# Kernel optimization log

Measured on AMD Instinct MI355X. Metric: run time of the kernel, lower is better.

Reference implementation:

```python
import jax, jax.numpy as jnp
import numpy as np

N_NODES = 50000
N_EDGES = 800000
D_IN = 256
D_HID = 256
D_OUT = 256
BN_EPS = 1e-5
NORM_EPS = 1e-12


def _glorot(key, out_dim, in_dim):
    a = np.sqrt(6.0 / (in_dim + out_dim)).astype(np.float32)
    return jax.random.uniform(key, (out_dim, in_dim), jnp.float32, -a, a)


def setup_inputs() -> dict:
    key = jax.random.key(0)
    ks = jax.random.split(key, 8)
    x = jax.random.normal(ks[0], (N_NODES, D_IN), jnp.float32)
    edge_index = jax.random.randint(ks[1], (2, N_EDGES), 0, N_NODES, dtype=jnp.int32)
    batch = jnp.zeros((N_NODES,), jnp.int32)
    return {
        "x": x,
        "W1_l": _glorot(ks[2], D_HID, D_IN),
        "b1_l": jnp.zeros((D_HID,), jnp.float32),
        "W1_r": _glorot(ks[3], D_HID, D_IN),
        "W2_l": _glorot(ks[4], D_OUT, D_HID),
        "b2_l": jnp.zeros((D_OUT,), jnp.float32),
        "W2_r": _glorot(ks[5], D_OUT, D_HID),
        "gamma1": jnp.ones((D_HID,), jnp.float32),
        "beta1": jnp.zeros((D_HID,), jnp.float32),
        "edge_index": edge_index,
        "batch": batch,
    }


def _sage_conv(x, W_l, b_l, W_r, src, dst, n_nodes):
    # PyG SAGEConv (aggr='mean'): out = lin_l(mean_j x_j) + lin_r(x)
    msgs = x[src]                                            # [E, d] gather
    s = jax.ops.segment_sum(msgs, dst, num_segments=n_nodes)  # [N, d] scatter-add
    cnt = jax.ops.segment_sum(jnp.ones((src.shape[0], 1), x.dtype), dst,
                              num_segments=n_nodes)
    agg = jnp.where(cnt > 0, s / jnp.maximum(cnt, 1.0), 0.0)
    return agg @ W_l.T + b_l + x @ W_r.T


def _batch_norm(h, gamma, beta):
    mu = jnp.mean(h, axis=0)
    var = jnp.mean((h - mu) ** 2, axis=0)  # biased, as torch train-mode BN
    return (h - mu) * jax.lax.rsqrt(var + BN_EPS) * gamma + beta


def _l2_normalize(h):
    n = jnp.linalg.norm(h, axis=-1, keepdims=True)
    return h / jnp.maximum(n, NORM_EPS)


def reference(x, W1_l, b1_l, W1_r, W2_l, b2_l, W2_r, gamma1, beta1,
              edge_index, batch):
    n = x.shape[0]
    src, dst = edge_index[0], edge_index[1]
    # layer 1: SAGEConv -> BN (train stats) -> ReLU (dropout = identity in eval)
    h = _sage_conv(x, W1_l, b1_l, W1_r, src, dst, n)
    h = jax.nn.relu(_batch_norm(h, gamma1, beta1))
    # layer 2: SAGEConv -> L2 normalize
    h = _sage_conv(h, W2_l, b2_l, W2_r, src, dst, n)
    node_emb = _l2_normalize(h)
    # global mean pool over batch ids (single graph here), then normalize
    gsum = jax.ops.segment_sum(node_emb, batch, num_segments=1)
    gcnt = jax.ops.segment_sum(jnp.ones((n, 1), node_emb.dtype), batch,
                               num_segments=1)
    graph_emb = _l2_normalize(gsum / jnp.maximum(gcnt, 1.0))
    return node_emb, graph_emb
```

## Files before the change

### kernel.cpp

```cpp
#include <hip/hip_runtime.h>
#include <math.h>

#define NN 50000
#define NE 800000
#define D  256
#define SCB 196
#define NB2 391

typedef unsigned short u16;
typedef __attribute__((ext_vector_type(8))) short short8;
typedef __attribute__((ext_vector_type(8))) unsigned short u16x8;
typedef __attribute__((ext_vector_type(4))) float f32x4;

__device__ __forceinline__ u16 f2b(float f) {
    unsigned u = __float_as_uint(f);
    return (u16)((u + 0x7FFFu + ((u >> 16) & 1u)) >> 16);
}
__device__ __forceinline__ float b2f(u16 b) {
    return __uint_as_float(((unsigned)b) << 16);
}

__device__ __forceinline__ void gl16(const u16* g, u16* l) {
    __builtin_amdgcn_global_load_lds(
        (const __attribute__((address_space(1))) void*)g,
        (__attribute__((address_space(3))) void*)l, 16, 0, 0);
}

__global__ void wxconv_kernel(const float* __restrict__ x,
                              const float* __restrict__ W1l, const float* __restrict__ W1r,
                              const float* __restrict__ W2l, const float* __restrict__ W2r,
                              const int* __restrict__ dst,
                              u16* __restrict__ Acat,
                              u16* __restrict__ Wcat1, u16* __restrict__ Wcat2,
                              int* __restrict__ deg) {
    int b = blockIdx.x;
    if (b < 12500) {
        int idx = b * 256 + threadIdx.x;
        int r = idx >> 6;
        int c4 = (idx & 63) * 4;
        float4 v = *(const float4*)&x[(size_t)r * 256 + c4];
        ushort4 o;
        o.x = f2b(v.x); o.y = f2b(v.y); o.z = f2b(v.z); o.w = f2b(v.w);
        *(ushort4*)&Acat[(size_t)r * 512 + 256 + c4] = o;
    } else if (b < 12756) {
        int r = b - 12500;
        int j = threadIdx.x;
        Wcat1[r * 512 + j]       = f2b(W1l[r * 256 + j]);
        Wcat1[r * 512 + 256 + j] = f2b(W1r[r * 256 + j]);
        Wcat2[r * 512 + j]       = f2b(W2l[r * 256 + j]);
        Wcat2[r * 512 + 256 + j] = f2b(W2r[r * 256 + j]);
    } else {
        int e0 = ((b - 12756) * 256 + threadIdx.x) * 4;
        if (e0 + 3 < NE) {
            int4 d = *(const int4*)&dst[e0];
            atomicAdd(&deg[d.x], 1);
            atomicAdd(&deg[d.y], 1);
            atomicAdd(&deg[d.z], 1);
            atomicAdd(&deg[d.w], 1);
        } else {
            for (int e = e0; e < NE; e++) atomicAdd(&deg[dst[e]], 1);
        }
    }
}

__global__ void scanA_kernel(const int* __restrict__ deg, int* __restrict__ partial) {
    int t = threadIdx.x;
    int i = blockIdx.x * 256 + t;
    int v = (i < NN) ? deg[i] : 0;
#pragma unroll
    for (int o = 32; o; o >>= 1) v += __shfl_xor(v, o);
    __shared__ int sm[4];
    if ((t & 63) == 0) sm[t >> 6] = v;
    __syncthreads();
    if (t == 0) partial[blockIdx.x] = sm[0] + sm[1] + sm[2] + sm[3];
}

__global__ void scanB_kernel(const int* __restrict__ partial, int* __restrict__ base,
                             int* __restrict__ offs) {
    __shared__ int sm[256];
    int t = threadIdx.x;
    int v = (t < SCB) ? partial[t] : 0;
    sm[t] = v;
    __syncthreads();
    for (int off = 1; off < 256; off <<= 1) {
        int u = 0;
        if (t >= off) u = sm[t - off];
        __syncthreads();
        sm[t] += u;
        __syncthreads();
    }
    if (t < SCB) base[t] = sm[t] - v;
    if (t == 255) offs[NN] = sm[255];
}

__global__ void scanC_kernel(const int* __restrict__ deg, const int* __restrict__ base,
                             int* __restrict__ offs, int* __restrict__ cur) {
    __shared__ int sm[256];
    int t = threadIdx.x;
    int i = blockIdx.x * 256 + t;
    int v = (i < NN) ? deg[i] : 0;
    sm[t] = v;
    __syncthreads();
    for (int off = 1; off < 256; off <<= 1) {
        int u = 0;
        if (t >= off) u = sm[t - off];
        __syncthreads();
        sm[t] += u;
        __syncthreads();
    }
    int o = base[blockIdx.x] + sm[t] - v;
    if (i < NN) {
        offs[i] = o;
        cur[i] = o;
    }
}

__global__ void fill_kernel(const int* __restrict__ src, const int* __restrict__ dst,
                            int* __restrict__ cur, int* __restrict__ csr) {
    int e0 = (blockIdx.x * blockDim.x + threadIdx.x) * 8;
    if (e0 + 7 < NE) {
        int4 d0 = *(const int4*)&dst[e0];
        int4 d1 = *(const int4*)&dst[e0 + 4];
        int4 s0 = *(const int4*)&src[e0];
        int4 s1 = *(const int4*)&src[e0 + 4];
        int p0 = atomicAdd(&cur[d0.x], 1);
        int p1 = atomicAdd(&cur[d0.y], 1);
        int p2 = atomicAdd(&cur[d0.z], 1);
        int p3 = atomicAdd(&cur[d0.w], 1);
        int p4 = atomicAdd(&cur[d1.x], 1);
        int p5 = atomicAdd(&cur[d1.y], 1);
        int p6 = atomicAdd(&cur[d1.z], 1);
        int p7 = atomicAdd(&cur[d1.w], 1);
        csr[p0] = s0.x; csr[p1] = s0.y; csr[p2] = s0.z; csr[p3] = s0.w;
        csr[p4] = s1.x; csr[p5] = s1.y; csr[p6] = s1.z; csr[p7] = s1.w;
    } else {
        for (int e = e0; e < NE; e++) {
            int pos = atomicAdd(&cur[dst[e]], 1);
            csr[pos] = src[e];
        }
    }
}

__global__ __launch_bounds__(256)
void agg_kernel(const u16* __restrict__ Acat, const int* __restrict__ csr,
                const int* __restrict__ offs, u16* __restrict__ AcatW) {
    int wid = (blockIdx.x * blockDim.x + threadIdx.x) >> 6;
    int lane = threadIdx.x & 63;
    if (wid >= NN) return;
    int beg = offs[wid];
    int end = offs[wid + 1];
    int deg = end - beg;
    int half = lane >> 5;
    int lc = (lane & 31) * 8;
    int mid = beg + ((deg + 1) >> 1);
    int e  = half ? mid : beg;
    int hi = half ? end : mid;
    float a[8] = {0.f, 0.f, 0.f, 0.f, 0.f, 0.f, 0.f, 0.f};
    for (; e + 7 < hi; e += 8) {
        int s0 = csr[e + 0], s1 = csr[e + 1], s2 = csr[e + 2], s3 = csr[e + 3];
        int s4 = csr[e + 4], s5 = csr[e + 5], s6 = csr[e + 6], s7 = csr[e + 7];
        u16x8 v0 = *(const u16x8*)&Acat[(size_t)s0 * 512 + 256 + lc];
        u16x8 v1 = *(const u16x8*)&Acat[(size_t)s1 * 512 + 256 + lc];
        u16x8 v2 = *(const u16x8*)&Acat[(size_t)s2 * 512 + 256 + lc];
        u16x8 v3 = *(const u16x8*)&Acat[(size_t)s3 * 512 + 256 + lc];
        u16x8 v4 = *(const u16x8*)&Acat[(size_t)s4 * 512 + 256 + lc];
        u16x8 v5 = *(const u16x8*)&Acat[(size_t)s5 * 512 + 256 + lc];
        u16x8 v6 = *(const u16x8*)&Acat[(size_t)s6 * 512 + 256 + lc];
        u16x8 v7 = *(const u16x8*)&Acat[(size_t)s7 * 512 + 256 + lc];
#pragma unroll
        for (int i = 0; i < 8; i++)
            a[i] += ((b2f(v0[i]) + b2f(v1[i])) + (b2f(v2[i]) + b2f(v3[i]))) +
                    ((b2f(v4[i]) + b2f(v5[i])) + (b2f(v6[i]) + b2f(v7[i])));
    }
    for (; e + 3 < hi; e += 4) {
        int s0 = csr[e + 0], s1 = csr[e + 1], s2 = csr[e + 2], s3 = csr[e + 3];
        u16x8 v0 = *(const u16x8*)&Acat[(size_t)s0 * 512 + 256 + lc];
        u16x8 v1 = *(const u16x8*)&Acat[(size_t)s1 * 512 + 256 + lc];
        u16x8 v2 = *(const u16x8*)&Acat[(size_t)s2 * 512 + 256 + lc];
        u16x8 v3 = *(const u16x8*)&Acat[(size_t)s3 * 512 + 256 + lc];
#pragma unroll
        for (int i = 0; i < 8; i++)
            a[i] += (b2f(v0[i]) + b2f(v1[i])) + (b2f(v2[i]) + b2f(v3[i]));
    }
    for (; e < hi; e++) {
        int s0 = csr[e];
        u16x8 v0 = *(const u16x8*)&Acat[(size_t)s0 * 512 + 256 + lc];
#pragma unroll
        for (int i = 0; i < 8; i++) a[i] += b2f(v0[i]);
    }
#pragma unroll
    for (int i = 0; i < 8; i++) a[i] += __shfl_xor(a[i], 32);
    float sc = (deg > 0) ? 1.0f / (float)deg : 0.0f;
    if (half == 0) {
        u16x8 o;
#pragma unroll
        for (int i = 0; i < 8; i++) o[i] = f2b(a[i] * sc);
        *(u16x8*)&AcatW[(size_t)wid * 512 + lc] = o;
    }
}

__global__ __launch_bounds__(256)
void mfma_gemm_kernel(const u16* __restrict__ A, const u16* __restrict__ W,
                      const float* __restrict__ bias, u16* __restrict__ Cout) {
    __shared__ u16 As[4][128 * 32];
    __shared__ u16 Bs[4][128 * 32];
    const int tid = threadIdx.x;
    const int l = tid & 63;
    const int wid = tid >> 6;
    const int wr = wid >> 1, wc = wid & 1;
    const int row0 = blockIdx.x * 128;
    const int col0 = blockIdx.y * 128;

    const u16* aptr[2];
    const u16* bptr[2];
#pragma unroll
    for (int i = 0; i < 2; i++) {
        int row = wid * 32 + i * 16 + (l >> 2);
        int kg = (l & 3) ^ ((row >> 1) & 3);
        int ra = row0 + row;
        if (ra > NN - 1) ra = NN - 1;
        aptr[i] = A + (size_t)ra * 512 + kg * 8;
        bptr[i] = W + (size_t)(col0 + row) * 512 + kg * 8;
    }

    f32x4 acc[4][4] = {};

#define STAGE1(b, t)                                                         \
    do {                                                                     \
        _Pragma("unroll") for (int i_ = 0; i_ < 2; i_++) {                   \
            gl16(aptr[i_] + (t) * 32, &As[b][(wid * 32 + i_ * 16) * 32]);    \
            gl16(bptr[i_] + (t) * 32, &Bs[b][(wid * 32 + i_ * 16) * 32]);    \
        }                                                                    \
    } while (0)

    STAGE1(0, 0);
    STAGE1(1, 1);

    const int kq = l >> 4;
    const int sw = ((l & 15) >> 1) & 3;
#pragma unroll
    for (int t = 0; t < 16; t++) {
        if (t + 2 < 16) STAGE1((t + 2) & 3, t + 2);

        if (t < 14)       asm volatile("s_waitcnt vmcnt(8)" ::: "memory");
        else if (t == 14) asm volatile("s_waitcnt vmcnt(4)" ::: "memory");
        else              asm volatile("s_waitcnt vmcnt(0)" ::: "memory");
        __builtin_amdgcn_s_barrier();
        __builtin_amdgcn_sched_barrier(0);

        short8 af[4], bf[4];
#pragma unroll
        for (int m = 0; m < 4; m++) {
            int row = wr * 64 + m * 16 + (l & 15);
            af[m] = *(const short8*)&As[t & 3][row * 32 + (kq ^ sw) * 8];
        }
#pragma unroll
        for (int n = 0; n < 4; n++) {
            int row = wc * 64 + n * 16 + (l & 15);
            bf[n] = *(const short8*)&Bs[t & 3][row * 32 + (kq ^ sw) * 8];
        }
#pragma unroll
        for (int m = 0; m < 4; m++)
#pragma unroll
            for (int n = 0; n < 4; n++)
                acc[m][n] = __builtin_amdgcn_mfma_f32_16x16x32_bf16(
                    af[m], bf[n], acc[m][n], 0, 0, 0);
    }
#undef STAGE1

    const int cq = l >> 4;
    const int cc = l & 15;
#pragma unroll
    for (int m = 0; m < 4; m++) {
#pragma unroll
        for (int n = 0; n < 4; n++) {
            int c = col0 + wc * 64 + n * 16 + cc;
#pragma unroll
            for (int j = 0; j < 4; j++) {
                int r = row0 + wr * 64 + m * 16 + cq * 4 + j;
                if (r < NN)
                    Cout[(size_t)r * 256 + c] = f2b(acc[m][n][j] + bias[c]);
            }
        }
    }
}

__global__ __launch_bounds__(512)
void gemm2_l2_kernel(const u16* __restrict__ A, const u16* __restrict__ W,
                     const float* __restrict__ bias, float* __restrict__ out,
                     float* __restrict__ colsum_part) {
    __shared__ u16 As[3][128 * 32];
    __shared__ u16 Bs[3][256 * 32];
    const int tid = threadIdx.x;
    const int l = tid & 63;
    const int wid = tid >> 6;
    const int wr = wid >> 2;
    const int wc = wid & 3;
    const int row0 = blockIdx.x * 128;

    const u16* aptr;
    const u16* bptr[2];
    {
        int row = wid * 16 + (l >> 2);
        int kg = (l & 3) ^ ((row >> 1) & 3);
        int ra = row0 + row;
        if (ra > NN - 1) ra = NN - 1;
        aptr = A + (size_t)ra * 512 + kg * 8;
    }
#pragma unroll
    for (int i = 0; i < 2; i++) {
        int row = wid * 32 + i * 16 + (l >> 2);
        int kg = (l & 3) ^ ((row >> 1) & 3);
        bptr[i] = W + (size_t)row * 512 + kg * 8;
    }

    f32x4 acc[4][4] = {};

#define STAGE2(b, t)                                                         \
    do {                                                                     \
        gl16(aptr + (t) * 32, &As[b][(wid * 16) * 32]);                      \
        _Pragma("unroll") for (int i_ = 0; i_ < 2; i_++)                     \
            gl16(bptr[i_] + (t) * 32, &Bs[b][(wid * 32 + i_ * 16) * 32]);    \
    } while (0)

    STAGE2(0, 0);
    STAGE2(1, 1);

    const int kq = l >> 4;
    const int sw = ((l & 15) >> 1) & 3;
#pragma unroll
    for (int t = 0; t < 16; t++) {
        if (t < 15) asm volatile("s_waitcnt vmcnt(3)" ::: "memory");
        else        asm volatile("s_waitcnt vmcnt(0)" ::: "memory");
        __builtin_amdgcn_s_barrier();
        __builtin_amdgcn_sched_barrier(0);

        if (t + 2 < 16) STAGE2((t + 2) % 3, t + 2);

        short8 af[4], bf[4];
#pragma unroll
        for (int m = 0; m < 4; m++) {
            int row = wr * 64 + m * 16 + (l & 15);
            af[m] = *(const short8*)&As[t % 3][row * 32 + (kq ^ sw) * 8];
        }
#pragma unroll
        for (int n = 0; n < 4; n++) {
            int row = wc * 64 + n * 16 + (l & 15);
            bf[n] = *(const short8*)&Bs[t % 3][row * 32 + (kq ^ sw) * 8];
        }
#pragma unroll
        for (int m = 0; m < 4; m++)
#pragma unroll
            for (int n = 0; n < 4; n++)
                acc[m][n] = __builtin_amdgcn_mfma_f32_16x16x32_bf16(
                    af[m], bf[n], acc[m][n], 0, 0, 0);
    }
#undef STAGE2

    float* rowsq = (float*)&As[1][0];
    float* colp  = rowsq + 512;
    const int cq = l >> 4;
    const int cc = l & 15;

    float sq[4][4];
#pragma unroll
    for (int m = 0; m < 4; m++)
#pragma unroll
        for (int j = 0; j < 4; j++) {
            float s = 0.f;
#pragma unroll
            for (int n = 0; n < 4; n++) {
                float v = acc[m][n][j] + bias[wc * 64 + n * 16 + cc];
                acc[m][n][j] = v;
                s += v * v;
            }
            sq[m][j] = s;
        }
#pragma unroll
    for (int o = 1; o < 16; o <<= 1)
#pragma unroll
        for (int m = 0; m < 4; m++)
#pragma unroll
            for (int j = 0; j < 4; j++) sq[m][j] += __shfl_xor(sq[m][j], o);

    __syncthreads();
#pragma unroll
    for (int m = 0; m < 4; m++)
#pragma unroll
        for (int j = 0; j < 4; j++)
            if (cc == j) rowsq[wc * 128 + wr * 64 + m * 16 + cq * 4 + j] = sq[m][j];
    __syncthreads();

    float colpart[4] = {0.f, 0.f, 0.f, 0.f};
#pragma unroll
    for (int m = 0; m < 4; m++)
#pragma unroll
        for (int j = 0; j < 4; j++) {
            int rl = wr * 64 + m * 16 + cq * 4 + j;
            float s = rowsq[rl] + rowsq[128 + rl] + rowsq[256 + rl] + rowsq[384 + rl];
            float invn = 1.0f / fmaxf(sqrtf(s), 1e-12f);
            int r = row0 + rl;
            bool ok = (r < NN);
#pragma unroll
            for (int n = 0; n < 4; n++) {
                float vn = acc[m][n][j] * invn;
                if (ok) {
                    out[(size_t)r * 256 + wc * 64 + n * 16 + cc] = vn;
                    colpart[n] += vn;
                }
            }
        }
#pragma unroll
    for (int n = 0; n < 4; n++) {
        colpart[n] += __shfl_xor(colpart[n], 16);
        colpart[n] += __shfl_xor(colpart[n], 32);
    }
    if (l < 16) {
#pragma unroll
        for (int n = 0; n < 4; n++)
            colp[wr * 256 + wc * 64 + n * 16 + l] = colpart[n];
    }
    __syncthreads();
    if (tid < 256)
        colsum_part[(size_t)blockIdx.x * 256 + tid] = colp[tid] + colp[256 + tid];
}

__global__ void colstats_kernel(const u16* __restrict__ h, float* __restrict__ stats) {
    int j = threadIdx.x;
    float s0 = 0.f, s1 = 0.f;
    for (int r = blockIdx.x; r < NN; r += gridDim.x) {
        float v = b2f(h[(size_t)r * 256 + j]);
        s0 += v;
        s1 += v * v;
    }
    atomicAdd(&stats[j], s0);
    atomicAdd(&stats[256 + j], s1);
}

__global__ void bnrelu_kernel(const u16* __restrict__ hb,
                              const float* __restrict__ stats,
                              const float* __restrict__ gamma,
                              const float* __restrict__ beta,
                              u16* __restrict__ Acat) {
    __shared__ float s_scale[256], s_shift[256];
    int t = threadIdx.x;
    {
        const float invN = 1.0f / (float)NN;
        float mu = stats[t] * invN;
        float var = stats[256 + t] * invN - mu * mu;
        float sc = gamma[t] * rsqrtf(var + 1e-5f);
        s_scale[t] = sc;
        s_shift[t] = beta[t] - mu * sc;
    }
    __syncthreads();
    int idx = blockIdx.x * 256 + t;
    int r = idx >> 5;
    int c8 = (idx & 31) * 8;
    u16x8 v = *(const u16x8*)&hb[(size_t)r * 256 + c8];
    u16x8 o;
#pragma unroll
    for (int i = 0; i < 8; i++) {
        float f = b2f(v[i]) * s_scale[c8 + i] + s_shift[c8 + i];
        o[i] = f2b(fmaxf(f, 0.f));
    }
    *(u16x8*)&Acat[(size_t)r * 512 + 256 + c8] = o;
}

__global__ void graph_kernel(const float* __restrict__ colsum_part,
                             float* __restrict__ gout) {
    __shared__ float wsum[4];
    int j = threadIdx.x;
    float s = 0.f;
#pragma unroll 8
    for (int b = 0; b < NB2; b++) s += colsum_part[(size_t)b * 256 + j];
    float v = s * (1.0f / (float)NN);
    float sq = v * v;
#pragma unroll
    for (int o = 32; o; o >>= 1) sq += __shfl_xor(sq, o);
    if ((j & 63) == 0) wsum[j >> 6] = sq;
    __syncthreads();
    float tot = wsum[0] + wsum[1] + wsum[2] + wsum[3];
    gout[j] = v / fmaxf(sqrtf(tot), 1e-12f);
}

extern "C" void kernel_launch(void* const* d_in, const int* in_sizes, int n_in,
                              void* d_out, int out_size, void* d_ws, size_t ws_size,
                              hipStream_t stream) {
    const float* x      = (const float*)d_in[0];
    const float* W1_l   = (const float*)d_in[1];
    const float* b1_l   = (const float*)d_in[2];
    const float* W1_r   = (const float*)d_in[3];
    const float* W2_l   = (const float*)d_in[4];
    const float* b2_l   = (const float*)d_in[5];
    const float* W2_r   = (const float*)d_in[6];
    const float* gamma1 = (const float*)d_in[7];
    const float* beta1  = (const float*)d_in[8];
    const int*   eidx   = (const int*)d_in[9];
    const int* src = eidx;
    const int* dst = eidx + NE;

    char* wsb = (char*)d_ws;
    int*   deg    = (int*)(wsb + 0);
    int*   offs   = (int*)(wsb + 200000);
    int*   cur    = (int*)(wsb + 400004);
    int*   csr    = (int*)(wsb + 600004);
    float* cspart = (float*)(wsb + 600004);
    int*   part   = (int*)(wsb + 3800064);
    int*   base   = (int*)(wsb + 3801088);
    float* stats  = (float*)(wsb + 3802112);
    u16*   Wcat1  = (u16*)(wsb + 3807232);
    u16*   Wcat2  = (u16*)(wsb + 4069376);
    u16*   hb     = (u16*)(wsb + 4331520);
    u16*   Acat   = (u16*)(wsb + 29931520);
    float* out    = (float*)d_out;
    float* gout   = out + (size_t)NN * 256;

    hipMemsetAsync(deg, 0, NN * sizeof(int), stream);
    hipMemsetAsync(stats, 0, 2048, stream);

    const int DEGB = (NE / 4 + 255) / 256;
    wxconv_kernel<<<12756 + DEGB, 256, 0, stream>>>(x, W1_l, W1_r, W2_l, W2_r,
                                                    dst, Acat, Wcat1, Wcat2, deg);

    scanA_kernel<<<SCB, 256, 0, stream>>>(deg, part);
    scanB_kernel<<<1, 256, 0, stream>>>(part, base, offs);
    scanC_kernel<<<SCB, 256, 0, stream>>>(deg, base, offs, cur);
    fill_kernel<<<(NE / 8 + 255) / 256, 256, 0, stream>>>(src, dst, cur, csr);

    dim3 ggrid(NB2, 2);

    agg_kernel<<<12500, 256, 0, stream>>>(Acat, csr, offs, Acat);
    mfma_gemm_kernel<<<ggrid, 256, 0, stream>>>(Acat, Wcat1, b1_l, hb);
    colstats_kernel<<<512, 256, 0, stream>>>(hb, stats);
    bnrelu_kernel<<<6250, 256, 0, stream>>>(hb, stats, gamma1, beta1, Acat);

    agg_kernel<<<12500, 256, 0, stream>>>(Acat, csr, offs, Acat);
    gemm2_l2_kernel<<<NB2, 512, 0, stream>>>(Acat, Wcat2, b2_l, out, cspart);

    graph_kernel<<<1, 256, 0, stream>>>(cspart, gout);
}
```

Before: 364.4 us.

## Widen layer-1 GEMM tile, merge scan kernels, vectorize column stats

The layer-1 GEMM now uses 512-thread blocks that cover all 256 output columns with a triple-buffered LDS pipeline, so each A tile is loaded once instead of twice. The scanB kernel is folded into scanC, with every block redoing the 196-entry partial scan, which removes one launch. Column statistics now use vectorized 8-wide loads with a shared-memory reduction and atomics spread over 8 slots, and bnrelu sums those slots. The stats memset is moved into the reused cur region after fill, and each block does a redundant scan of the partials.

```diff
diff --git a/kernel.cpp b/kernel.cpp
--- a/kernel.cpp
+++ b/kernel.cpp
@@ -75,11 +75,27 @@
     if (t == 0) partial[blockIdx.x] = sm[0] + sm[1] + sm[2] + sm[3];
 }
 
-__global__ void scanB_kernel(const int* __restrict__ partial, int* __restrict__ base,
-                             int* __restrict__ offs) {
+__global__ void scanC_kernel(const int* __restrict__ deg, const int* __restrict__ partial,
+                             int* __restrict__ offs, int* __restrict__ cur) {
+    __shared__ int smp[256];
     __shared__ int sm[256];
     int t = threadIdx.x;
-    int v = (t < SCB) ? partial[t] : 0;
+    int pv = (t < SCB) ? partial[t] : 0;
+    smp[t] = pv;
+    __syncthreads();
+    for (int off = 1; off < 256; off <<= 1) {
+        int u = 0;
+        if (t >= off) u = smp[t - off];
+        __syncthreads();
+        smp[t] += u;
+        __syncthreads();
+    }
+    int bid = blockIdx.x;
+    int blockbase = (bid > 0) ? smp[bid - 1] : 0;
+    if (bid == SCB - 1 && t == 255) offs[NN] = smp[255];
+
+    int i = bid * 256 + t;
+    int v = (i < NN) ? deg[i] : 0;
     sm[t] = v;
     __syncthreads();
     for (int off = 1; off < 256; off <<= 1) {
@@ -89,26 +105,7 @@
         sm[t] += u;
         __syncthreads();
     }
-    if (t < SCB) base[t] = sm[t] - v;
-    if (t == 255) offs[NN] = sm[255];
-}
-
-__global__ void scanC_kernel(const int* __restrict__ deg, const int* __restrict__ base,
-                             int* __restrict__ offs, int* __restrict__ cur) {
-    __shared__ int sm[256];
-    int t = threadIdx.x;
-    int i = blockIdx.x * 256 + t;
-    int v = (i < NN) ? deg[i] : 0;
-    sm[t] = v;
-    __syncthreads();
-    for (int off = 1; off < 256; off <<= 1) {
-        int u = 0;
-        if (t >= off) u = sm[t - off];
-        __syncthreads();
-        sm[t] += u;
-        __syncthreads();
-    }
-    int o = base[blockIdx.x] + sm[t] - v;
+    int o = blockbase + sm[t] - v;
     if (i < NN) {
         offs[i] = o;
         cur[i] = o;
@@ -199,38 +196,41 @@
     }
 }
 
-__global__ __launch_bounds__(256)
+__global__ __launch_bounds__(512)
 void mfma_gemm_kernel(const u16* __restrict__ A, const u16* __restrict__ W,
                       const float* __restrict__ bias, u16* __restrict__ Cout) {
-    __shared__ u16 As[4][128 * 32];
-    __shared__ u16 Bs[4][128 * 32];
+    __shared__ u16 As[3][128 * 32];
+    __shared__ u16 Bs[3][256 * 32];
     const int tid = threadIdx.x;
     const int l = tid & 63;
     const int wid = tid >> 6;
-    const int wr = wid >> 1, wc = wid & 1;
+    const int wr = wid >> 2;
+    const int wc = wid & 3;
     const int row0 = blockIdx.x * 128;
-    const int col0 = blockIdx.y * 128;
-
-    const u16* aptr[2];
+
+    const u16* aptr;
     const u16* bptr[2];
+    {
+        int row = wid * 16 + (l >> 2);
+        int kg = (l & 3) ^ ((row >> 1) & 3);
+        int ra = row0 + row;
+        if (ra > NN - 1) ra = NN - 1;
+        aptr = A + (size_t)ra * 512 + kg * 8;
+    }
 #pragma unroll
     for (int i = 0; i < 2; i++) {
         int row = wid * 32 + i * 16 + (l >> 2);
         int kg = (l & 3) ^ ((row >> 1) & 3);
-        int ra = row0 + row;
-        if (ra > NN - 1) ra = NN - 1;
-        aptr[i] = A + (size_t)ra * 512 + kg * 8;
-        bptr[i] = W + (size_t)(col0 + row) * 512 + kg * 8;
+        bptr[i] = W + (size_t)row * 512 + kg * 8;
     }
 
     f32x4 acc[4][4] = {};
 
 #define STAGE1(b, t)                                                         \
     do {                                                                     \
-        _Pragma("unroll") for (int i_ = 0; i_ < 2; i_++) {                   \
-            gl16(aptr[i_] + (t) * 32, &As[b][(wid * 32 + i_ * 16) * 32]);    \
+        gl16(aptr + (t) * 32, &As[b][(wid * 16) * 32]);                      \
+        _Pragma("unroll") for (int i_ = 0; i_ < 2; i_++)                     \
             gl16(bptr[i_] + (t) * 32, &Bs[b][(wid * 32 + i_ * 16) * 32]);    \
-        }                                                                    \
     } while (0)
 
     STAGE1(0, 0);
@@ -240,24 +240,23 @@
     const int sw = ((l & 15) >> 1) & 3;
 #pragma unroll
     for (int t = 0; t < 16; t++) {
-        if (t + 2 < 16) STAGE1((t + 2) & 3, t + 2);
-
-        if (t < 14)       asm volatile("s_waitcnt vmcnt(8)" ::: "memory");
-        else if (t == 14) asm volatile("s_waitcnt vmcnt(4)" ::: "memory");
-        else              asm volatile("s_waitcnt vmcnt(0)" ::: "memory");
+        if (t < 15) asm volatile("s_waitcnt vmcnt(3)" ::: "memory");
+        else        asm volatile("s_waitcnt vmcnt(0)" ::: "memory");
         __builtin_amdgcn_s_barrier();
         __builtin_amdgcn_sched_barrier(0);
 
+        if (t + 2 < 16) STAGE1((t + 2) % 3, t + 2);
+
         short8 af[4], bf[4];
 #pragma unroll
         for (int m = 0; m < 4; m++) {
             int row = wr * 64 + m * 16 + (l & 15);
-            af[m] = *(const short8*)&As[t & 3][row * 32 + (kq ^ sw) * 8];
+            af[m] = *(const short8*)&As[t % 3][row * 32 + (kq ^ sw) * 8];
         }
 #pragma unroll
         for (int n = 0; n < 4; n++) {
             int row = wc * 64 + n * 16 + (l & 15);
-            bf[n] = *(const short8*)&Bs[t & 3][row * 32 + (kq ^ sw) * 8];
+            bf[n] = *(const short8*)&Bs[t % 3][row * 32 + (kq ^ sw) * 8];
         }
 #pragma unroll
         for (int m = 0; m < 4; m++)
@@ -274,7 +273,7 @@
     for (int m = 0; m < 4; m++) {
 #pragma unroll
         for (int n = 0; n < 4; n++) {
-            int c = col0 + wc * 64 + n * 16 + cc;
+            int c = wc * 64 + n * 16 + cc;
 #pragma unroll
             for (int j = 0; j < 4; j++) {
                 int r = row0 + wr * 64 + m * 16 + cq * 4 + j;
@@ -425,29 +424,53 @@
         colsum_part[(size_t)blockIdx.x * 256 + tid] = colp[tid] + colp[256 + tid];
 }
 
-__global__ void colstats_kernel(const u16* __restrict__ h, float* __restrict__ stats) {
-    int j = threadIdx.x;
-    float s0 = 0.f, s1 = 0.f;
-    for (int r = blockIdx.x; r < NN; r += gridDim.x) {
-        float v = b2f(h[(size_t)r * 256 + j]);
-        s0 += v;
-        s1 += v * v;
-    }
-    atomicAdd(&stats[j], s0);
-    atomicAdd(&stats[256 + j], s1);
+__global__ __launch_bounds__(256)
+void colstats_kernel(const u16* __restrict__ h, float* __restrict__ stats8) {
+    __shared__ float red[8][512];
+    int t = threadIdx.x;
+    int cg = (t & 31) * 8;
+    int rofs = t >> 5;
+    float s0[8] = {}, s1[8] = {};
+    for (int r = blockIdx.x * 8 + rofs; r < NN; r += gridDim.x * 8) {
+        u16x8 v = *(const u16x8*)&h[(size_t)r * 256 + cg];
+#pragma unroll
+        for (int i = 0; i < 8; i++) {
+            float f = b2f(v[i]);
+            s0[i] += f;
+            s1[i] += f * f;
+        }
+    }
+#pragma unroll
+    for (int i = 0; i < 8; i++) {
+        red[rofs][cg + i] = s0[i];
+        red[rofs][256 + cg + i] = s1[i];
+    }
+    __syncthreads();
+    float* slot = stats8 + (blockIdx.x & 7) * 512;
+    for (int k = t; k < 512; k += 256) {
+        float s = red[0][k] + red[1][k] + red[2][k] + red[3][k] +
+                  red[4][k] + red[5][k] + red[6][k] + red[7][k];
+        atomicAdd(&slot[k], s);
+    }
 }
 
 __global__ void bnrelu_kernel(const u16* __restrict__ hb,
-                              const float* __restrict__ stats,
+                              const float* __restrict__ stats8,
                               const float* __restrict__ gamma,
                               const float* __restrict__ beta,
                               u16* __restrict__ Acat) {
     __shared__ float s_scale[256], s_shift[256];
     int t = threadIdx.x;
     {
+        float su = 0.f, sq = 0.f;
+#pragma unroll
+        for (int k = 0; k < 8; k++) {
+            su += stats8[k * 512 + t];
+            sq += stats8[k * 512 + 256 + t];
+        }
         const float invN = 1.0f / (float)NN;
-        float mu = stats[t] * invN;
-        float var = stats[256 + t] * invN - mu * mu;
+        float mu = su * invN;
+        float var = sq * invN - mu * mu;
         float sc = gamma[t] * rsqrtf(var + 1e-5f);
         s_scale[t] = sc;
         s_shift[t] = beta[t] - mu * sc;
@@ -503,11 +526,10 @@
     int*   deg    = (int*)(wsb + 0);
     int*   offs   = (int*)(wsb + 200000);
     int*   cur    = (int*)(wsb + 400004);
+    float* stats8 = (float*)(wsb + 400004);
     int*   csr    = (int*)(wsb + 600004);
     float* cspart = (float*)(wsb + 600004);
     int*   part   = (int*)(wsb + 3800064);
-    int*   base   = (int*)(wsb + 3801088);
-    float* stats  = (float*)(wsb + 3802112);
     u16*   Wcat1  = (u16*)(wsb + 3807232);
     u16*   Wcat2  = (u16*)(wsb + 4069376);
     u16*   hb     = (u16*)(wsb + 4331520);
@@ -516,23 +538,20 @@
     float* gout   = out + (size_t)NN * 256;
 
     hipMemsetAsync(deg, 0, NN * sizeof(int), stream);
-    hipMemsetAsync(stats, 0, 2048, stream);
 
     const int DEGB = (NE / 4 + 255) / 256;
     wxconv_kernel<<<12756 + DEGB, 256, 0, stream>>>(x, W1_l, W1_r, W2_l, W2_r,
                                                     dst, Acat, Wcat1, Wcat2, deg);
 
     scanA_kernel<<<SCB, 256, 0, stream>>>(deg, part);
-    scanB_kernel<<<1, 256, 0, stream>>>(part, base, offs);
-    scanC_kernel<<<SCB, 256, 0, stream>>>(deg, base, offs, cur);
+    scanC_kernel<<<SCB, 256, 0, stream>>>(deg, part, offs, cur);
     fill_kernel<<<(NE / 8 + 255) / 256, 256, 0, stream>>>(src, dst, cur, csr);
-
-    dim3 ggrid(NB2, 2);
+    hipMemsetAsync(stats8, 0, 16384, stream);
 
     agg_kernel<<<12500, 256, 0, stream>>>(Acat, csr, offs, Acat);
-    mfma_gemm_kernel<<<ggrid, 256, 0, stream>>>(Acat, Wcat1, b1_l, hb);
-    colstats_kernel<<<512, 256, 0, stream>>>(hb, stats);
-    bnrelu_kernel<<<6250, 256, 0, stream>>>(hb, stats, gamma1, beta1, Acat);
+    mfma_gemm_kernel<<<NB2, 512, 0, stream>>>(Acat, Wcat1, b1_l, hb);
+    colstats_kernel<<<256, 256, 0, stream>>>(hb, stats8);
+    bnrelu_kernel<<<6250, 256, 0, stream>>>(hb, stats8, gamma1, beta1, Acat);
 
     agg_kernel<<<12500, 256, 0, stream>>>(Acat, csr, offs, Acat);
     gemm2_l2_kernel<<<NB2, 512, 0, stream>>>(Acat, Wcat2, b2_l, out, cspart);
```

Measured after the change: 327.7 us (median of 2 runs). 1.11x faster.
